# Kernel tuning notes

Hardware: AMD Instinct MI355X
Metric: run time of the kernel (lower is better)

Reference implementation:

```python
import jax, jax.numpy as jnp
import numpy as np

B = 512          # batch size (<= 640 so the original's %640 on row indices is a no-op)
FEATS = 30       # active HalfKP features per position (max pieces minus kings)
NNZ = B * FEATS
FT_OUT = 512
N_FEAT = 40960
N_VFEAT = 640


def setup_inputs() -> dict:
    key = jax.random.key(0)
    ks = jax.random.split(key, 8)
    rows = jnp.repeat(jnp.arange(B, dtype=jnp.int32), FEATS)  # COO batch-row ids
    stm_cols = jax.random.randint(ks[0], (NNZ,), 0, N_FEAT, dtype=jnp.int32)
    nstm_cols = jax.random.randint(ks[1], (NNZ,), 0, N_FEAT, dtype=jnp.int32)
    stm_indices = jnp.stack([rows, stm_cols])    # [2, NNZ]
    nstm_indices = jnp.stack([rows, nstm_cols])  # [2, NNZ]
    values = jnp.ones((NNZ,), jnp.float32)       # NNUE features are 0/1
    s_ft = 1.0 / np.sqrt(N_FEAT)
    s_fft = 1.0 / np.sqrt(N_VFEAT)
    s_out = 1.0 / np.sqrt(2 * FT_OUT)
    return {
        'stm_indices': stm_indices,
        'nstm_indices': nstm_indices,
        'values': values,
        'ft_w': jax.random.normal(ks[2], (FT_OUT, N_FEAT), jnp.float32) * s_ft,
        'ft_b': jax.random.normal(ks[3], (FT_OUT,), jnp.float32) * s_ft,
        'fft_w': jax.random.normal(ks[4], (FT_OUT, N_VFEAT), jnp.float32) * s_fft,
        'fft_b': jax.random.normal(ks[5], (FT_OUT,), jnp.float32) * s_fft,
        'out_w': jax.random.normal(ks[6], (1, 2 * FT_OUT), jnp.float32) * s_out,
        'out_b': jax.random.normal(ks[7], (1,), jnp.float32) * s_out,
    }


def reference(stm_indices, nstm_indices, values, ft_w, ft_b, fft_w, fft_b, out_w, out_b):
    ft_wt = ft_w.T    # [N_FEAT, FT_OUT]
    fft_wt = fft_w.T  # [N_VFEAT, FT_OUT]

    def half_ft(idx):
        # sparse COO (rows, cols) embedding-bag: gather weight columns, scale, segment-sum per row
        rows, cols = idx[0], idx[1]
        g = ft_wt[cols] * values[:, None]            # real HalfKP features
        gv = fft_wt[cols % N_VFEAT] * values[:, None]  # factorized 'virtual' features
        acc = jax.ops.segment_sum(g + gv, rows, num_segments=B)  # [B, FT_OUT]
        return acc + ft_b + fft_b

    stm_ft = half_ft(stm_indices)
    nstm_ft = half_ft(nstm_indices)
    hidden = jnp.clip(jnp.concatenate([stm_ft, nstm_ft], axis=1), 0.0, 1.0)
    return jax.nn.sigmoid(hidden @ out_w.T + out_b)  # [B, 1]
```

## Files before the change

### kernel.cpp

```cpp
#include <hip/hip_runtime.h>
#include <math.h>

#define BATCH   512
#define FEATS   30
#define NNZT    (BATCH * FEATS)
#define FT_OUT  512
#define NFEAT   40960
#define NVFEAT  640

#define FT_TILES  ((FT_OUT / 64) * (NFEAT / 64))
#define FFT_TILES ((FT_OUT / 64) * (NVFEAT / 64))
#define NTILES    (FT_TILES + FFT_TILES)

__device__ inline unsigned int bpack(float a, float b) {
    unsigned int ua = __float_as_uint(a), ub = __float_as_uint(b);
    ua = (ua + 0x7fff + ((ua >> 16) & 1)) >> 16;
    ub = (ub + 0x7fff + ((ub >> 16) & 1)) >> 16;
    return ua | (ub << 16);
}
__device__ inline float bf2f(unsigned int u) {
    return __uint_as_float(u << 16);
}
__device__ inline float bf2f_hi(unsigned int u) {
    return __uint_as_float(u & 0xffff0000u);
}

__global__ __launch_bounds__(256) void transpose_pack(
    const float* __restrict__ ft_w, const float* __restrict__ fft_w,
    unsigned short* __restrict__ ftT, unsigned short* __restrict__ fftT)
{
    __shared__ float tile[64][65];
    const int wid  = threadIdx.x >> 6;
    const int lane = threadIdx.x & 63;
    const int t = blockIdx.x;

    const float* W; unsigned short* T; int C, fb, cb;
    if (t < FT_TILES) {
        W = ft_w;  T = ftT;  C = NFEAT;
        fb = (t & 7) * 64;  cb = (t >> 3) * 64;
    } else {
        int u = t - FT_TILES;
        W = fft_w; T = fftT; C = NVFEAT;
        fb = (u & 7) * 64;  cb = (u >> 3) * 64;
    }

#pragma unroll
    for (int it = 0; it < 4; ++it) {
        const int row = it * 16 + wid * 4 + (lane >> 4);
        const int cq  = (lane & 15) * 4;
        const float4 v = *(const float4*)(W + (size_t)(fb + row) * C + cb + cq);
        tile[cq + 0][row] = v.x;
        tile[cq + 1][row] = v.y;
        tile[cq + 2][row] = v.z;
        tile[cq + 3][row] = v.w;
    }
    __syncthreads();

#pragma unroll
    for (int it = 0; it < 2; ++it) {
        const int c  = it * 32 + (threadIdx.x >> 3);
        const int f0 = (threadIdx.x & 7) * 8;
        uint4 o;
        unsigned int* op = (unsigned int*)&o;
#pragma unroll
        for (int j = 0; j < 4; ++j)
            op[j] = bpack(tile[c][f0 + 2 * j], tile[c][f0 + 2 * j + 1]);
        *(uint4*)(T + (size_t)(cb + c) * FT_OUT + fb + f0) = o;
    }
}

__global__ __launch_bounds__(512) void gather_out(
    const unsigned short* __restrict__ ftT,
    const unsigned short* __restrict__ fftT,
    const int*   __restrict__ stm_idx,
    const int*   __restrict__ nstm_idx,
    const float* __restrict__ values,
    const float* __restrict__ ft_b, const float* __restrict__ fft_b,
    const float* __restrict__ out_w, const float* __restrict__ out_b,
    float*       __restrict__ out)
{
    __shared__ int   cs[2][FEATS];
    __shared__ float vs[FEATS];
    __shared__ float pacc[8][2][FT_OUT];
    __shared__ float red[8];

    const int b    = blockIdx.x;
    const int wid  = threadIdx.x >> 6;
    const int lane = threadIdx.x & 63;

    if (threadIdx.x < FEATS)
        cs[0][threadIdx.x] = stm_idx[NNZT + b * FEATS + threadIdx.x];
    else if (threadIdx.x < 2 * FEATS)
        cs[1][threadIdx.x - FEATS] = nstm_idx[NNZT + b * FEATS + (threadIdx.x - FEATS)];
    else if (threadIdx.x < 3 * FEATS)
        vs[threadIdx.x - 2 * FEATS] = values[b * FEATS + (threadIdx.x - 2 * FEATS)];
    __syncthreads();

    const int f0 = lane * 8;
    float a0[8], a1[8];
#pragma unroll
    for (int i = 0; i < 8; ++i) { a0[i] = 0.0f; a1[i] = 0.0f; }

    for (int k = wid; k < 4 * FEATS; k += 8) {
        const int h = k >= 2 * FEATS;
        const int j = k - h * 2 * FEATS;
        const int jj = (j >= FEATS) ? j - FEATS : j;
        const int c = cs[h][jj];
        const float v = vs[jj];
        const unsigned short* rowp = (j >= FEATS)
            ? fftT + (size_t)(c % NVFEAT) * FT_OUT
            : ftT  + (size_t)c * FT_OUT;
        const uint4 r = *(const uint4*)(rowp + f0);
        const unsigned int* rw = (const unsigned int*)&r;
        float* acc = h ? a1 : a0;
#pragma unroll
        for (int q = 0; q < 4; ++q) {
            acc[2 * q]     += bf2f(rw[q]) * v;
            acc[2 * q + 1] += bf2f_hi(rw[q]) * v;
        }
    }

#pragma unroll
    for (int i = 0; i < 8; i += 4) {
        *(float4*)&pacc[wid][0][f0 + i] = make_float4(a0[i], a0[i+1], a0[i+2], a0[i+3]);
        *(float4*)&pacc[wid][1][f0 + i] = make_float4(a1[i], a1[i+1], a1[i+2], a1[i+3]);
    }
    __syncthreads();

    const int f = threadIdx.x;
    float s0 = 0.0f, s1 = 0.0f;
#pragma unroll
    for (int w = 0; w < 8; ++w) { s0 += pacc[w][0][f]; s1 += pacc[w][1][f]; }

    const float bias = ft_b[f] + fft_b[f];
    const float h0 = fminf(fmaxf(s0 + bias, 0.0f), 1.0f);
    const float h1 = fminf(fmaxf(s1 + bias, 0.0f), 1.0f);

    float total = h0 * out_w[f] + h1 * out_w[FT_OUT + f];
#pragma unroll
    for (int off = 32; off > 0; off >>= 1)
        total += __shfl_down(total, off, 64);
    if (lane == 0) red[wid] = total;
    __syncthreads();
    if (threadIdx.x == 0) {
        float s = red[0];
#pragma unroll
        for (int w = 1; w < 8; ++w) s += red[w];
        s += out_b[0];
        out[b] = 1.0f / (1.0f + expf(-s));
    }
}

__global__ __launch_bounds__(512) void halfkp_direct(
    const int* __restrict__ stm_idx, const int* __restrict__ nstm_idx,
    const float* __restrict__ values,
    const float* __restrict__ ft_w, const float* __restrict__ ft_b,
    const float* __restrict__ fft_w, const float* __restrict__ fft_b,
    const float* __restrict__ out_w, const float* __restrict__ out_b,
    float* __restrict__ out)
{
    const int b = blockIdx.x;
    const int f = threadIdx.x;
    const float bias = ft_b[f] + fft_b[f];
    const float* ftrow  = ft_w  + (size_t)f * NFEAT;
    const float* fftrow = fft_w + f * NVFEAT;
    float acc0 = bias, acc1 = bias;
    for (int k = 0; k < FEATS; ++k) {
        int j = b * FEATS + k;
        int c0 = stm_idx[NNZT + j], c1 = nstm_idx[NNZT + j];
        float v = values[j];
        acc0 += (ftrow[c0] + fftrow[c0 % NVFEAT]) * v;
        acc1 += (ftrow[c1] + fftrow[c1 % NVFEAT]) * v;
    }
    const float h0 = fminf(fmaxf(acc0, 0.0f), 1.0f);
    const float h1 = fminf(fmaxf(acc1, 0.0f), 1.0f);
    float total = h0 * out_w[f] + h1 * out_w[FT_OUT + f];
#pragma unroll
    for (int off = 32; off > 0; off >>= 1)
        total += __shfl_down(total, off, 64);
    __shared__ float red[8];
    if ((threadIdx.x & 63) == 0) red[threadIdx.x >> 6] = total;
    __syncthreads();
    if (threadIdx.x == 0) {
        float s = red[0];
#pragma unroll
        for (int w = 1; w < 8; ++w) s += red[w];
        out[b] = 1.0f / (1.0f + expf(-(s + out_b[0])));
    }
}

extern "C" void kernel_launch(void* const* d_in, const int* in_sizes, int n_in,
                              void* d_out, int out_size, void* d_ws, size_t ws_size,
                              hipStream_t stream)
{
    const int*   stm_idx  = (const int*)  d_in[0];
    const int*   nstm_idx = (const int*)  d_in[1];
    const float* values   = (const float*)d_in[2];
    const float* ft_w     = (const float*)d_in[3];
    const float* ft_b     = (const float*)d_in[4];
    const float* fft_w    = (const float*)d_in[5];
    const float* fft_b    = (const float*)d_in[6];
    const float* out_w    = (const float*)d_in[7];
    const float* out_b    = (const float*)d_in[8];
    float*       out      = (float*)d_out;

    const size_t ftT_bytes  = (size_t)NFEAT  * FT_OUT * 2;
    const size_t fftT_bytes = (size_t)NVFEAT * FT_OUT * 2;

    if (ws_size >= ftT_bytes + fftT_bytes) {
        unsigned short* ftT  = (unsigned short*)d_ws;
        unsigned short* fftT = (unsigned short*)((char*)d_ws + ftT_bytes);

        transpose_pack<<<NTILES, 256, 0, stream>>>(ft_w, fft_w, ftT, fftT);
        gather_out<<<BATCH, 512, 0, stream>>>(ftT, fftT, stm_idx, nstm_idx,
                                              values, ft_b, fft_b, out_w, out_b, out);
    } else {
        halfkp_direct<<<BATCH, 512, 0, stream>>>(stm_idx, nstm_idx, values,
                                                 ft_w, ft_b, fft_w, fft_b,
                                                 out_w, out_b, out);
    }
}
```

Baseline: 156.2 us.

## Fuse transpose-pack and gather into one cooperative kernel with grid sync

Merges the weight transpose/bf16-pack kernel and the per-batch gather kernel into a single cooperative launch of 512 blocks. Each block first transposes two tiles at a time in a grid-stride loop, then all blocks wait on a grid-wide barrier before doing the gather and output reduction, reusing the same shared memory for both phases. This removes one kernel launch and its tail. In exchange the transpose runs on only 512 resident blocks instead of thousands of small ones, and it adds the cost of the grid-wide barrier.

```diff
diff --git a/kernel.cpp b/kernel.cpp
--- a/kernel.cpp
+++ b/kernel.cpp
@@ -1,5 +1,8 @@
 #include <hip/hip_runtime.h>
+#include <hip/hip_cooperative_groups.h>
 #include <math.h>
+
+namespace cg = cooperative_groups;
 
 #define BATCH   512
 #define FEATS   30
@@ -11,6 +14,7 @@
 #define FT_TILES  ((FT_OUT / 64) * (NFEAT / 64))
 #define FFT_TILES ((FT_OUT / 64) * (NVFEAT / 64))
 #define NTILES    (FT_TILES + FFT_TILES)
+#define NPAIRS    (NTILES / 2)
 
 __device__ inline unsigned int bpack(float a, float b) {
     unsigned int ua = __float_as_uint(a), ub = __float_as_uint(b);
@@ -25,75 +29,83 @@
     return __uint_as_float(u & 0xffff0000u);
 }
 
-__global__ __launch_bounds__(256) void transpose_pack(
-    const float* __restrict__ ft_w, const float* __restrict__ fft_w,
-    unsigned short* __restrict__ ftT, unsigned short* __restrict__ fftT)
-{
-    __shared__ float tile[64][65];
-    const int wid  = threadIdx.x >> 6;
-    const int lane = threadIdx.x & 63;
-    const int t = blockIdx.x;
-
-    const float* W; unsigned short* T; int C, fb, cb;
-    if (t < FT_TILES) {
-        W = ft_w;  T = ftT;  C = NFEAT;
-        fb = (t & 7) * 64;  cb = (t >> 3) * 64;
-    } else {
-        int u = t - FT_TILES;
-        W = fft_w; T = fftT; C = NVFEAT;
-        fb = (u & 7) * 64;  cb = (u >> 3) * 64;
-    }
-
-#pragma unroll
-    for (int it = 0; it < 4; ++it) {
-        const int row = it * 16 + wid * 4 + (lane >> 4);
-        const int cq  = (lane & 15) * 4;
-        const float4 v = *(const float4*)(W + (size_t)(fb + row) * C + cb + cq);
-        tile[cq + 0][row] = v.x;
-        tile[cq + 1][row] = v.y;
-        tile[cq + 2][row] = v.z;
-        tile[cq + 3][row] = v.w;
-    }
-    __syncthreads();
-
-#pragma unroll
-    for (int it = 0; it < 2; ++it) {
-        const int c  = it * 32 + (threadIdx.x >> 3);
-        const int f0 = (threadIdx.x & 7) * 8;
-        uint4 o;
-        unsigned int* op = (unsigned int*)&o;
-#pragma unroll
-        for (int j = 0; j < 4; ++j)
-            op[j] = bpack(tile[c][f0 + 2 * j], tile[c][f0 + 2 * j + 1]);
-        *(uint4*)(T + (size_t)(cb + c) * FT_OUT + fb + f0) = o;
-    }
-}
-
-__global__ __launch_bounds__(512) void gather_out(
-    const unsigned short* __restrict__ ftT,
-    const unsigned short* __restrict__ fftT,
+__global__ __launch_bounds__(512) void halfkp_fused(
+    unsigned short* __restrict__ ftT,
+    unsigned short* __restrict__ fftT,
     const int*   __restrict__ stm_idx,
     const int*   __restrict__ nstm_idx,
     const float* __restrict__ values,
+    const float* __restrict__ ft_w,
+    const float* __restrict__ fft_w,
     const float* __restrict__ ft_b, const float* __restrict__ fft_b,
     const float* __restrict__ out_w, const float* __restrict__ out_b,
     float*       __restrict__ out)
 {
+    __shared__ float smem[2 * 64 * 65];
     __shared__ int   cs[2][FEATS];
     __shared__ float vs[FEATS];
-    __shared__ float pacc[8][2][FT_OUT];
     __shared__ float red[8];
 
-    const int b    = blockIdx.x;
-    const int wid  = threadIdx.x >> 6;
-    const int lane = threadIdx.x & 63;
-
-    if (threadIdx.x < FEATS)
-        cs[0][threadIdx.x] = stm_idx[NNZT + b * FEATS + threadIdx.x];
-    else if (threadIdx.x < 2 * FEATS)
-        cs[1][threadIdx.x - FEATS] = nstm_idx[NNZT + b * FEATS + (threadIdx.x - FEATS)];
-    else if (threadIdx.x < 3 * FEATS)
-        vs[threadIdx.x - 2 * FEATS] = values[b * FEATS + (threadIdx.x - 2 * FEATS)];
+    const int tid  = threadIdx.x;
+    const int half = tid >> 8;
+    const int htid = tid & 255;
+    const int wid4 = htid >> 6;
+    const int lane = tid & 63;
+
+    float (*tileh)[65] = (float (*)[65])(smem + half * 64 * 65);
+
+    for (int p = blockIdx.x; p < NPAIRS; p += gridDim.x) {
+        const int t = 2 * p + half;
+
+        const float* W; unsigned short* T; int C, fb, cb;
+        if (t < FT_TILES) {
+            W = ft_w;  T = ftT;  C = NFEAT;
+            fb = (t & 7) * 64;  cb = (t >> 3) * 64;
+        } else {
+            int u = t - FT_TILES;
+            W = fft_w; T = fftT; C = NVFEAT;
+            fb = (u & 7) * 64;  cb = (u >> 3) * 64;
+        }
+
+#pragma unroll
+        for (int it = 0; it < 4; ++it) {
+            const int row = it * 16 + wid4 * 4 + (lane >> 4);
+            const int cq  = (lane & 15) * 4;
+            const float4 v = *(const float4*)(W + (size_t)(fb + row) * C + cb + cq);
+            tileh[cq + 0][row] = v.x;
+            tileh[cq + 1][row] = v.y;
+            tileh[cq + 2][row] = v.z;
+            tileh[cq + 3][row] = v.w;
+        }
+        __syncthreads();
+
+#pragma unroll
+        for (int it = 0; it < 2; ++it) {
+            const int c  = it * 32 + (htid >> 3);
+            const int f0 = (htid & 7) * 8;
+            uint4 o;
+            unsigned int* op = (unsigned int*)&o;
+#pragma unroll
+            for (int j = 0; j < 4; ++j)
+                op[j] = bpack(tileh[c][f0 + 2 * j], tileh[c][f0 + 2 * j + 1]);
+            *(uint4*)(T + (size_t)(cb + c) * FT_OUT + fb + f0) = o;
+        }
+        __syncthreads();
+    }
+
+    cg::this_grid().sync();
+
+    float (*pacc)[2][FT_OUT] = (float (*)[2][FT_OUT])smem;
+
+    const int b   = blockIdx.x;
+    const int wid = tid >> 6;
+
+    if (tid < FEATS)
+        cs[0][tid] = stm_idx[NNZT + b * FEATS + tid];
+    else if (tid < 2 * FEATS)
+        cs[1][tid - FEATS] = nstm_idx[NNZT + b * FEATS + (tid - FEATS)];
+    else if (tid < 3 * FEATS)
+        vs[tid - 2 * FEATS] = values[b * FEATS + (tid - 2 * FEATS)];
     __syncthreads();
 
     const int f0 = lane * 8;
@@ -127,7 +139,7 @@
     }
     __syncthreads();
 
-    const int f = threadIdx.x;
+    const int f = tid;
     float s0 = 0.0f, s1 = 0.0f;
 #pragma unroll
     for (int w = 0; w < 8; ++w) { s0 += pacc[w][0][f]; s1 += pacc[w][1][f]; }
@@ -142,7 +154,7 @@
         total += __shfl_down(total, off, 64);
     if (lane == 0) red[wid] = total;
     __syncthreads();
-    if (threadIdx.x == 0) {
+    if (tid == 0) {
         float s = red[0];
 #pragma unroll
         for (int w = 1; w < 8; ++w) s += red[w];
@@ -211,9 +223,15 @@
         unsigned short* ftT  = (unsigned short*)d_ws;
         unsigned short* fftT = (unsigned short*)((char*)d_ws + ftT_bytes);
 
-        transpose_pack<<<NTILES, 256, 0, stream>>>(ft_w, fft_w, ftT, fftT);
-        gather_out<<<BATCH, 512, 0, stream>>>(ftT, fftT, stm_idx, nstm_idx,
-                                              values, ft_b, fft_b, out_w, out_b, out);
+        void* args[] = {
+            (void*)&ftT, (void*)&fftT,
+            (void*)&stm_idx, (void*)&nstm_idx, (void*)&values,
+            (void*)&ft_w, (void*)&fft_w,
+            (void*)&ft_b, (void*)&fft_b,
+            (void*)&out_w, (void*)&out_b, (void*)&out
+        };
+        hipLaunchCooperativeKernel((const void*)halfkp_fused,
+                                   dim3(BATCH), dim3(512), args, 0, stream);
     } else {
         halfkp_direct<<<BATCH, 512, 0, stream>>>(stm_idx, nstm_idx, values,
                                                  ft_w, ft_b, fft_w, fft_b,
```

Result: slower. 233.7 us (+49.7%).
